# Kernel optimization log

Measured on AMD Instinct MI355X. Metric: run time of the kernel, lower is better.

The kernel has to match this reference:

```python
import jax, jax.numpy as jnp
import numpy as np

EPS = 1e-8
Q_MAX = 127.0  # 2**(8-1) - 1


def _activation_quant(x):
    gamma = jnp.maximum(jnp.max(jnp.abs(x)), EPS)
    scale = Q_MAX / gamma
    x_int = jnp.clip(jnp.round(x * scale), -Q_MAX, Q_MAX)
    x_fq = x_int / scale
    # straight-through estimator
    return x + jax.lax.stop_gradient(x_fq - x)


def _weight_quant(w):
    gamma = jnp.maximum(jnp.mean(jnp.abs(w)), EPS)
    w_int = jnp.clip(jnp.round(w / gamma), -1.0, 1.0)
    w_fq = w_int * gamma
    return w + jax.lax.stop_gradient(w_fq - w)


def setup_inputs() -> dict:
    key = jax.random.key(0)
    kx, kw, kb = jax.random.split(key, 3)
    in_features, out_features = 2048, 2048
    x = jax.random.normal(kx, (4, 4096, in_features), dtype=jnp.float32)
    # nn.Linear default init: U(-1/sqrt(fan_in), 1/sqrt(fan_in))
    bound = 1.0 / np.sqrt(in_features)
    W = jax.random.uniform(kw, (out_features, in_features), dtype=jnp.float32,
                           minval=-bound, maxval=bound)
    b = jax.random.uniform(kb, (out_features,), dtype=jnp.float32,
                           minval=-bound, maxval=bound)
    return {"x": x, "W": W, "b": b}


def reference(x, W, b):
    x_q = _activation_quant(x)          # int8 absmax fake-quant
    w_q = _weight_quant(W)              # ternary {-g, 0, g} fake-quant
    # F.linear: x @ W^T + b
    return jnp.einsum('bsi,oi->bso', x_q, w_q) + b
```

## Files before the change

kernel.cpp:

```cpp
#include <hip/hip_runtime.h>
#include <hip/hip_bf16.h>
#include <stdint.h>

typedef __attribute__((ext_vector_type(4))) int i32x4;

static constexpr long M_ = 16384;
static constexpr long N_ = 2048;
static constexpr long K_ = 2048;


#define GLOAD_LDS16(g, l)                                                          \
  __builtin_amdgcn_global_load_lds(                                               \
      (const __attribute__((address_space(1))) unsigned int*)(g),                 \
      (__attribute__((address_space(3))) unsigned int*)(l), 16, 0, 0)

__global__ __launch_bounds__(256) void k_stats(const float4* __restrict__ x,
                                               const float4* __restrict__ w,
                                               unsigned* __restrict__ gx_bits,
                                               double* __restrict__ gw_sum) {
  const int b = blockIdx.x;
  const int lane = threadIdx.x & 63, wv = threadIdx.x >> 6;
  if (b < 2048) {
    const long S = 524288;
    long i = (long)b * 256 + threadIdx.x;
    float m0 = 0.f, m1 = 0.f, m2 = 0.f, m3 = 0.f;
#pragma unroll
    for (int it = 0; it < 4; ++it) {
      float4 v0 = x[i];
      float4 v1 = x[i + S];
      float4 v2 = x[i + 2 * S];
      float4 v3 = x[i + 3 * S];
      m0 = fmaxf(m0, fmaxf(fmaxf(fabsf(v0.x), fabsf(v0.y)), fmaxf(fabsf(v0.z), fabsf(v0.w))));
      m1 = fmaxf(m1, fmaxf(fmaxf(fabsf(v1.x), fabsf(v1.y)), fmaxf(fabsf(v1.z), fabsf(v1.w))));
      m2 = fmaxf(m2, fmaxf(fmaxf(fabsf(v2.x), fabsf(v2.y)), fmaxf(fabsf(v2.z), fabsf(v2.w))));
      m3 = fmaxf(m3, fmaxf(fmaxf(fabsf(v3.x), fabsf(v3.y)), fmaxf(fabsf(v3.z), fabsf(v3.w))));
      i += 4 * S;
    }
    float m = fmaxf(fmaxf(m0, m1), fmaxf(m2, m3));
#pragma unroll
    for (int off = 32; off > 0; off >>= 1) m = fmaxf(m, __shfl_down(m, off));
    __shared__ float sm[4];
    if (lane == 0) sm[wv] = m;
    __syncthreads();
    if (threadIdx.x == 0) {
      float bm = fmaxf(fmaxf(sm[0], sm[1]), fmaxf(sm[2], sm[3]));
      atomicMax(gx_bits, __float_as_uint(bm));
    }
  } else {
    const long S = 131072;
    long i = (long)(b - 2048) * 256 + threadIdx.x;
    double s = 0.0;
#pragma unroll
    for (int it = 0; it < 8; ++it) {
      float4 v = w[i];
      s += (double)fabsf(v.x) + (double)fabsf(v.y) + (double)fabsf(v.z) + (double)fabsf(v.w);
      i += S;
    }
#pragma unroll
    for (int off = 32; off > 0; off >>= 1) s += __shfl_down(s, off);
    __shared__ double sd[4];
    if (lane == 0) sd[wv] = s;
    __syncthreads();
    if (threadIdx.x == 0) atomicAdd(gw_sum, (sd[0] + sd[1]) + (sd[2] + sd[3]));
  }
}

__global__ __launch_bounds__(256) void k_quant(const float4* __restrict__ x,
                                               const float4* __restrict__ w,
                                               char4* __restrict__ xq,
                                               char4* __restrict__ wq,
                                               const unsigned* __restrict__ gx_bits,
                                               const double* __restrict__ gw_sum) {
  const int b = blockIdx.x;
  if (b < 2048) {
    const double gx = (double)fmaxf(__uint_as_float(*gx_bits), 1e-8f);
    const double scale = 127.0 / gx;
    const long S = 524288;
    long i = (long)b * 256 + threadIdx.x;
#pragma unroll
    for (int it = 0; it < 16; ++it) {
      float4 v = x[i];
      char4 o;
      o.x = (signed char)(int)fmin(fmax(rint((double)v.x * scale), -127.0), 127.0);
      o.y = (signed char)(int)fmin(fmax(rint((double)v.y * scale), -127.0), 127.0);
      o.z = (signed char)(int)fmin(fmax(rint((double)v.z * scale), -127.0), 127.0);
      o.w = (signed char)(int)fmin(fmax(rint((double)v.w * scale), -127.0), 127.0);
      xq[i] = o;
      i += S;
    }
  } else {
    const double gw = fmax(*gw_sum * (1.0 / 4194304.0), 1e-8);
    const double inv = 1.0 / gw;
    const long S = 131072;
    long i = (long)(b - 2048) * 256 + threadIdx.x;
#pragma unroll
    for (int it = 0; it < 8; ++it) {
      float4 v = w[i];
      char4 o;
      o.x = (signed char)(int)fmin(fmax(rint((double)v.x * inv), -1.0), 1.0);
      o.y = (signed char)(int)fmin(fmax(rint((double)v.y * inv), -1.0), 1.0);
      o.z = (signed char)(int)fmin(fmax(rint((double)v.z * inv), -1.0), 1.0);
      o.w = (signed char)(int)fmin(fmax(rint((double)v.w * inv), -1.0), 1.0);
      wq[i] = o;
      i += S;
    }
  }
}


template <int P>
__device__ __forceinline__ void phaseP(signed char* lds, const signed char* Ap,
                                       const signed char* Bp, int kb,
                                       const signed char* pA, const signed char* pB,
                                       int go0, int ldsl0, i32x4 (&aS)[2][4],
                                       i32x4 (&bS)[2][4], i32x4 (&acc)[8][4]) {
  constexpr int Q = (P + 1) & 7;
  constexpr int QR = ((Q >> 2) & 1) * 32768 + ((Q >> 1) & 1) * 16384;
  constexpr int QMH = Q & 1;
#pragma unroll
  for (int m = 0; m < 4; ++m)
    aS[Q & 1][m] = *(const i32x4*)(pA + QR + QMH * 4096 + m * 1024);
  if constexpr (QMH == 0) {
#pragma unroll
    for (int n = 0; n < 4; ++n)
      bS[(Q >> 1) & 1][n] = *(const i32x4*)(pB + QR + n * 1024);
  }
  constexpr int SREG = ((P >> 1) + 3) & 3;
  constexpr int SOFF = ((SREG >> 1) & 1) * 32768 + (SREG & 1) * 16384;
  if constexpr ((P & 1) == 0) {
    GLOAD_LDS16(Ap + kb + go0, lds + SOFF + ldsl0);
    GLOAD_LDS16(Ap + kb + go0 + 32768, lds + SOFF + ldsl0 + 1024);
  } else {
    GLOAD_LDS16(Bp + kb + go0, lds + 65536 + SOFF + ldsl0);
    GLOAD_LDS16(Bp + kb + go0 + 32768, lds + 65536 + SOFF + ldsl0 + 1024);
  }
  __builtin_amdgcn_s_setprio(1);
#pragma unroll
  for (int m = 0; m < 4; ++m)
#pragma unroll
    for (int n = 0; n < 4; ++n)
      acc[(P & 1) * 4 + m][n] = __builtin_amdgcn_mfma_i32_16x16x64_i8(
          aS[P & 1][m], bS[(P >> 1) & 1][n], acc[(P & 1) * 4 + m][n], 0, 0, 0);
  __builtin_amdgcn_s_setprio(0);
  if constexpr ((P & 1) == 1) asm volatile("s_waitcnt vmcnt(4)" ::: "memory");
  __builtin_amdgcn_s_barrier();
}

__global__ __launch_bounds__(512, 2) void k_gemm(
    const signed char* __restrict__ Aq, const signed char* __restrict__ Bq,
    const float* __restrict__ bias, float* __restrict__ out,
    const unsigned* __restrict__ gx_bits, const double* __restrict__ gw_sum) {
  extern __shared__ signed char lds[];

  const int tid = threadIdx.x;
  const int lane = tid & 63;
  const int wid = tid >> 6;
  const int wave_m = wid >> 2;
  const int wave_n = wid & 3;
  const int l15 = lane & 15;

  const int wg = (int)((blockIdx.x & 7) * 64 + (blockIdx.x >> 3));
  const int nblk = wg & 7;
  const int mblk = wg >> 3;
  const long brow = (long)mblk * 256;
  const long bcol = (long)nblk * 256;

  const signed char* Ap = Aq + brow * K_;
  const signed char* Bp = Bq + bcol * K_;

  const int swz = ((lane >> 4) ^ ((l15 >> 1) & 3)) << 4;
  const signed char* pA = lds + (wave_m * 128 + l15) * 64 + swz;
  const signed char* pB = lds + 65536 + (wave_n * 64 + l15) * 64 + swz;

  const int c0 = (lane & 3) ^ ((lane >> 3) & 3);
  const int go0 = (wid * 32 + (lane >> 2)) * (int)K_ + c0 * 16;
  const int ldsl0 = wid * 2048;

  i32x4 acc[8][4];
#pragma unroll
  for (int m = 0; m < 8; m++)
#pragma unroll
    for (int n = 0; n < 4; n++) acc[m][n] = (i32x4){0, 0, 0, 0};
  i32x4 aS[2][4], bS[2][4];

  GLOAD_LDS16(Ap + go0, lds + ldsl0);
  GLOAD_LDS16(Ap + go0 + 32768, lds + ldsl0 + 1024);
  GLOAD_LDS16(Bp + go0, lds + 65536 + ldsl0);
  GLOAD_LDS16(Bp + go0 + 32768, lds + 65536 + ldsl0 + 1024);
  GLOAD_LDS16(Ap + 64 + go0, lds + 16384 + ldsl0);
  GLOAD_LDS16(Ap + 64 + go0 + 32768, lds + 16384 + ldsl0 + 1024);
  GLOAD_LDS16(Bp + 64 + go0, lds + 65536 + 16384 + ldsl0);
  GLOAD_LDS16(Bp + 64 + go0 + 32768, lds + 65536 + 16384 + ldsl0 + 1024);
  GLOAD_LDS16(Ap + 128 + go0, lds + 32768 + ldsl0);
  GLOAD_LDS16(Ap + 128 + go0 + 32768, lds + 32768 + ldsl0 + 1024);
  GLOAD_LDS16(Bp + 128 + go0, lds + 65536 + 32768 + ldsl0);
  GLOAD_LDS16(Bp + 128 + go0 + 32768, lds + 65536 + 32768 + ldsl0 + 1024);
  asm volatile("s_waitcnt vmcnt(0)" ::: "memory");
  __builtin_amdgcn_s_barrier();

#pragma unroll
  for (int n = 0; n < 4; ++n) bS[0][n] = *(const i32x4*)(pB + n * 1024);
#pragma unroll
  for (int m = 0; m < 4; ++m) aS[0][m] = *(const i32x4*)(pA + m * 1024);

  for (int kt = 0; kt < (int)K_; kt += 256) {
    const int c0k = (kt + 192) & 2047;
    const int c1k = (kt + 256) & 2047;
    const int c2k = (kt + 320) & 2047;
    const int c3k = (kt + 384) & 2047;
    phaseP<0>(lds, Ap, Bp, c0k, pA, pB, go0, ldsl0, aS, bS, acc);
    phaseP<1>(lds, Ap, Bp, c0k, pA, pB, go0, ldsl0, aS, bS, acc);
    phaseP<2>(lds, Ap, Bp, c1k, pA, pB, go0, ldsl0, aS, bS, acc);
    phaseP<3>(lds, Ap, Bp, c1k, pA, pB, go0, ldsl0, aS, bS, acc);
    phaseP<4>(lds, Ap, Bp, c2k, pA, pB, go0, ldsl0, aS, bS, acc);
    phaseP<5>(lds, Ap, Bp, c2k, pA, pB, go0, ldsl0, aS, bS, acc);
    phaseP<6>(lds, Ap, Bp, c3k, pA, pB, go0, ldsl0, aS, bS, acc);
    phaseP<7>(lds, Ap, Bp, c3k, pA, pB, go0, ldsl0, aS, bS, acc);
  }

  const float gxf = fmaxf(__uint_as_float(*gx_bits), 1e-8f);
  const double gwd = fmax(*gw_sum * (1.0 / 4194304.0), 1e-8);
  const float alpha = (float)((double)gxf * gwd * (1.0 / 127.0));

#pragma unroll
  for (int n = 0; n < 4; ++n) {
    const long col = bcol + wave_n * 64 + n * 16 + l15;
    const float bv = bias[col];
#pragma unroll
    for (int m = 0; m < 8; ++m) {
      const long row0 = brow + wave_m * 128 + m * 16 + (lane >> 4) * 4;
#pragma unroll
      for (int r = 0; r < 4; ++r) {
        out[(row0 + r) * N_ + col] = (float)acc[m][n][r] * alpha + bv;
      }
    }
  }
}

extern "C" void kernel_launch(void* const* d_in, const int* in_sizes, int n_in,
                              void* d_out, int out_size, void* d_ws, size_t ws_size,
                              hipStream_t stream) {
  const float* x = (const float*)d_in[0];
  const float* W = (const float*)d_in[1];
  const float* b = (const float*)d_in[2];
  float* out = (float*)d_out;

  char* ws = (char*)d_ws;
  double* gw_sum = (double*)ws;
  unsigned* gx_bits = (unsigned*)(ws + 8);
  signed char* xq = (signed char*)(ws + 256);
  signed char* wq = (signed char*)(ws + 256 + (size_t)M_ * (size_t)K_);

  static bool attr_set = false;
  if (!attr_set) {
    (void)hipFuncSetAttribute(reinterpret_cast<const void*>(&k_gemm),
                              hipFuncAttributeMaxDynamicSharedMemorySize, 131072);
    attr_set = true;
  }

  hipMemsetAsync(ws, 0, 16, stream);
  hipLaunchKernelGGL(k_stats, dim3(2560), dim3(256), 0, stream,
                     (const float4*)x, (const float4*)W, gx_bits, gw_sum);
  hipLaunchKernelGGL(k_quant, dim3(2560), dim3(256), 0, stream,
                     (const float4*)x, (const float4*)W, (char4*)xq, (char4*)wq,
                     gx_bits, gw_sum);
  hipLaunchKernelGGL(k_gemm, dim3((unsigned)((M_ / 256) * (N_ / 256))), dim3(512),
                     131072, stream, xq, wq, b, out, gx_bits, gw_sum);
}
```

Before: 156.6 us.

## Load A operand directly from global into registers, stage only B in LDS

The GEMM now reads the int8 activation fragments straight from global memory into registers, addressed per lane, and keeps only the weight tile in LDS. This halves LDS use (131072 to 65536 bytes), removes LDS traffic for A and drops the explicit vmcnt wait. The quant kernel also writes 16-byte vectors of int8 per thread instead of 4-byte char4 stores. The risk is that un-staged A loads are exposed to global latency and are no longer shared across the four waves in a row, raising L2/global traffic; the sync removal and sched_barrier change the ordering of memory and MFMA instructions.

```diff
diff --git a/kernel.cpp b/kernel.cpp
--- a/kernel.cpp
+++ b/kernel.cpp
@@ -67,73 +67,77 @@
 
 __global__ __launch_bounds__(256) void k_quant(const float4* __restrict__ x,
                                                const float4* __restrict__ w,
-                                               char4* __restrict__ xq,
-                                               char4* __restrict__ wq,
+                                               int4* __restrict__ xq,
+                                               int4* __restrict__ wq,
                                                const unsigned* __restrict__ gx_bits,
                                                const double* __restrict__ gw_sum) {
   const int b = blockIdx.x;
   if (b < 2048) {
     const double gx = (double)fmaxf(__uint_as_float(*gx_bits), 1e-8f);
     const double scale = 127.0 / gx;
-    const long S = 524288;
-    long i = (long)b * 256 + threadIdx.x;
-#pragma unroll
-    for (int it = 0; it < 16; ++it) {
-      float4 v = x[i];
-      char4 o;
-      o.x = (signed char)(int)fmin(fmax(rint((double)v.x * scale), -127.0), 127.0);
-      o.y = (signed char)(int)fmin(fmax(rint((double)v.y * scale), -127.0), 127.0);
-      o.z = (signed char)(int)fmin(fmax(rint((double)v.z * scale), -127.0), 127.0);
-      o.w = (signed char)(int)fmin(fmax(rint((double)v.w * scale), -127.0), 127.0);
-      xq[i] = o;
-      i += S;
+    const long G = 2048L * 256;
+    long t = (long)b * 256 + threadIdx.x;
+#pragma unroll
+    for (int it = 0; it < 4; ++it) {
+      signed char o[16];
+#pragma unroll
+      for (int q = 0; q < 4; ++q) {
+        float4 v = x[t * 4 + q];
+        o[q * 4 + 0] = (signed char)(int)fmin(fmax(rint((double)v.x * scale), -127.0), 127.0);
+        o[q * 4 + 1] = (signed char)(int)fmin(fmax(rint((double)v.y * scale), -127.0), 127.0);
+        o[q * 4 + 2] = (signed char)(int)fmin(fmax(rint((double)v.z * scale), -127.0), 127.0);
+        o[q * 4 + 3] = (signed char)(int)fmin(fmax(rint((double)v.w * scale), -127.0), 127.0);
+      }
+      xq[t] = *(const int4*)o;
+      t += G;
     }
   } else {
     const double gw = fmax(*gw_sum * (1.0 / 4194304.0), 1e-8);
     const double inv = 1.0 / gw;
-    const long S = 131072;
-    long i = (long)(b - 2048) * 256 + threadIdx.x;
-#pragma unroll
-    for (int it = 0; it < 8; ++it) {
-      float4 v = w[i];
-      char4 o;
-      o.x = (signed char)(int)fmin(fmax(rint((double)v.x * inv), -1.0), 1.0);
-      o.y = (signed char)(int)fmin(fmax(rint((double)v.y * inv), -1.0), 1.0);
-      o.z = (signed char)(int)fmin(fmax(rint((double)v.z * inv), -1.0), 1.0);
-      o.w = (signed char)(int)fmin(fmax(rint((double)v.w * inv), -1.0), 1.0);
-      wq[i] = o;
-      i += S;
+    const long G = 512L * 256;
+    long t = (long)(b - 2048) * 256 + threadIdx.x;
+#pragma unroll
+    for (int it = 0; it < 2; ++it) {
+      signed char o[16];
+#pragma unroll
+      for (int q = 0; q < 4; ++q) {
+        float4 v = w[t * 4 + q];
+        o[q * 4 + 0] = (signed char)(int)fmin(fmax(rint((double)v.x * inv), -1.0), 1.0);
+        o[q * 4 + 1] = (signed char)(int)fmin(fmax(rint((double)v.y * inv), -1.0), 1.0);
+        o[q * 4 + 2] = (signed char)(int)fmin(fmax(rint((double)v.z * inv), -1.0), 1.0);
+        o[q * 4 + 3] = (signed char)(int)fmin(fmax(rint((double)v.w * inv), -1.0), 1.0);
+      }
+      wq[t] = *(const int4*)o;
+      t += G;
     }
   }
 }
 
 
 template <int P>
-__device__ __forceinline__ void phaseP(signed char* lds, const signed char* Ap,
-                                       const signed char* Bp, int kb,
-                                       const signed char* pA, const signed char* pB,
-                                       int go0, int ldsl0, i32x4 (&aS)[2][4],
-                                       i32x4 (&bS)[2][4], i32x4 (&acc)[8][4]) {
+__device__ __forceinline__ void phaseP(signed char* lds, const signed char* Abase,
+                                       const signed char* Bp, int kA, int kb,
+                                       const signed char* pB, int go0, int ldsl0,
+                                       i32x4 (&aS)[2][4], i32x4 (&bS)[2][4],
+                                       i32x4 (&acc)[8][4]) {
   constexpr int Q = (P + 1) & 7;
-  constexpr int QR = ((Q >> 2) & 1) * 32768 + ((Q >> 1) & 1) * 16384;
   constexpr int QMH = Q & 1;
-#pragma unroll
-  for (int m = 0; m < 4; ++m)
-    aS[Q & 1][m] = *(const i32x4*)(pA + QR + QMH * 4096 + m * 1024);
+  const signed char* pa = Abase + QMH * 131072 + kA;
+#pragma unroll
+  for (int m = 0; m < 4; ++m) aS[Q & 1][m] = *(const i32x4*)(pa + m * 32768);
   if constexpr (QMH == 0) {
+    constexpr int QR = ((Q >> 2) & 1) * 32768 + ((Q >> 1) & 1) * 16384;
 #pragma unroll
     for (int n = 0; n < 4; ++n)
       bS[(Q >> 1) & 1][n] = *(const i32x4*)(pB + QR + n * 1024);
   }
-  constexpr int SREG = ((P >> 1) + 3) & 3;
-  constexpr int SOFF = ((SREG >> 1) & 1) * 32768 + (SREG & 1) * 16384;
   if constexpr ((P & 1) == 0) {
-    GLOAD_LDS16(Ap + kb + go0, lds + SOFF + ldsl0);
-    GLOAD_LDS16(Ap + kb + go0 + 32768, lds + SOFF + ldsl0 + 1024);
-  } else {
-    GLOAD_LDS16(Bp + kb + go0, lds + 65536 + SOFF + ldsl0);
-    GLOAD_LDS16(Bp + kb + go0 + 32768, lds + 65536 + SOFF + ldsl0 + 1024);
-  }
+    constexpr int SREG = ((P >> 1) + 3) & 3;
+    constexpr int SOFF = ((SREG >> 1) & 1) * 32768 + (SREG & 1) * 16384;
+    GLOAD_LDS16(Bp + kb + go0, lds + SOFF + ldsl0);
+    GLOAD_LDS16(Bp + kb + go0 + 32768, lds + SOFF + ldsl0 + 1024);
+  }
+  __builtin_amdgcn_sched_barrier(0);
   __builtin_amdgcn_s_setprio(1);
 #pragma unroll
   for (int m = 0; m < 4; ++m)
@@ -142,7 +146,6 @@
       acc[(P & 1) * 4 + m][n] = __builtin_amdgcn_mfma_i32_16x16x64_i8(
           aS[P & 1][m], bS[(P >> 1) & 1][n], acc[(P & 1) * 4 + m][n], 0, 0, 0);
   __builtin_amdgcn_s_setprio(0);
-  if constexpr ((P & 1) == 1) asm volatile("s_waitcnt vmcnt(4)" ::: "memory");
   __builtin_amdgcn_s_barrier();
 }
 
@@ -165,12 +168,12 @@
   const long brow = (long)mblk * 256;
   const long bcol = (long)nblk * 256;
 
-  const signed char* Ap = Aq + brow * K_;
+  const signed char* Abase =
+      Aq + (brow + wave_m * 128 + l15) * K_ + (lane >> 4) * 16;
   const signed char* Bp = Bq + bcol * K_;
 
   const int swz = ((lane >> 4) ^ ((l15 >> 1) & 3)) << 4;
-  const signed char* pA = lds + (wave_m * 128 + l15) * 64 + swz;
-  const signed char* pB = lds + 65536 + (wave_n * 64 + l15) * 64 + swz;
+  const signed char* pB = lds + (wave_n * 64 + l15) * 64 + swz;
 
   const int c0 = (lane & 3) ^ ((lane >> 3) & 3);
   const int go0 = (wid * 32 + (lane >> 2)) * (int)K_ + c0 * 16;
@@ -183,39 +186,29 @@
     for (int n = 0; n < 4; n++) acc[m][n] = (i32x4){0, 0, 0, 0};
   i32x4 aS[2][4], bS[2][4];
 
-  GLOAD_LDS16(Ap + go0, lds + ldsl0);
-  GLOAD_LDS16(Ap + go0 + 32768, lds + ldsl0 + 1024);
-  GLOAD_LDS16(Bp + go0, lds + 65536 + ldsl0);
-  GLOAD_LDS16(Bp + go0 + 32768, lds + 65536 + ldsl0 + 1024);
-  GLOAD_LDS16(Ap + 64 + go0, lds + 16384 + ldsl0);
-  GLOAD_LDS16(Ap + 64 + go0 + 32768, lds + 16384 + ldsl0 + 1024);
-  GLOAD_LDS16(Bp + 64 + go0, lds + 65536 + 16384 + ldsl0);
-  GLOAD_LDS16(Bp + 64 + go0 + 32768, lds + 65536 + 16384 + ldsl0 + 1024);
-  GLOAD_LDS16(Ap + 128 + go0, lds + 32768 + ldsl0);
-  GLOAD_LDS16(Ap + 128 + go0 + 32768, lds + 32768 + ldsl0 + 1024);
-  GLOAD_LDS16(Bp + 128 + go0, lds + 65536 + 32768 + ldsl0);
-  GLOAD_LDS16(Bp + 128 + go0 + 32768, lds + 65536 + 32768 + ldsl0 + 1024);
+  GLOAD_LDS16(Bp + go0, lds + ldsl0);
+  GLOAD_LDS16(Bp + go0 + 32768, lds + ldsl0 + 1024);
+  GLOAD_LDS16(Bp + 64 + go0, lds + 16384 + ldsl0);
+  GLOAD_LDS16(Bp + 64 + go0 + 32768, lds + 16384 + ldsl0 + 1024);
+  GLOAD_LDS16(Bp + 128 + go0, lds + 32768 + ldsl0);
+  GLOAD_LDS16(Bp + 128 + go0 + 32768, lds + 32768 + ldsl0 + 1024);
   asm volatile("s_waitcnt vmcnt(0)" ::: "memory");
   __builtin_amdgcn_s_barrier();
 
 #pragma unroll
   for (int n = 0; n < 4; ++n) bS[0][n] = *(const i32x4*)(pB + n * 1024);
 #pragma unroll
-  for (int m = 0; m < 4; ++m) aS[0][m] = *(const i32x4*)(pA + m * 1024);
+  for (int m = 0; m < 4; ++m) aS[0][m] = *(const i32x4*)(Abase + m * 32768);
 
   for (int kt = 0; kt < (int)K_; kt += 256) {
-    const int c0k = (kt + 192) & 2047;
-    const int c1k = (kt + 256) & 2047;
-    const int c2k = (kt + 320) & 2047;
-    const int c3k = (kt + 384) & 2047;
-    phaseP<0>(lds, Ap, Bp, c0k, pA, pB, go0, ldsl0, aS, bS, acc);
-    phaseP<1>(lds, Ap, Bp, c0k, pA, pB, go0, ldsl0, aS, bS, acc);
-    phaseP<2>(lds, Ap, Bp, c1k, pA, pB, go0, ldsl0, aS, bS, acc);
-    phaseP<3>(lds, Ap, Bp, c1k, pA, pB, go0, ldsl0, aS, bS, acc);
-    phaseP<4>(lds, Ap, Bp, c2k, pA, pB, go0, ldsl0, aS, bS, acc);
-    phaseP<5>(lds, Ap, Bp, c2k, pA, pB, go0, ldsl0, aS, bS, acc);
-    phaseP<6>(lds, Ap, Bp, c3k, pA, pB, go0, ldsl0, aS, bS, acc);
-    phaseP<7>(lds, Ap, Bp, c3k, pA, pB, go0, ldsl0, aS, bS, acc);
+    phaseP<0>(lds, Abase, Bp, (kt + 0) & 2047, (kt + 192) & 2047, pB, go0, ldsl0, aS, bS, acc);
+    phaseP<1>(lds, Abase, Bp, (kt + 64) & 2047, 0, pB, go0, ldsl0, aS, bS, acc);
+    phaseP<2>(lds, Abase, Bp, (kt + 64) & 2047, (kt + 256) & 2047, pB, go0, ldsl0, aS, bS, acc);
+    phaseP<3>(lds, Abase, Bp, (kt + 128) & 2047, 0, pB, go0, ldsl0, aS, bS, acc);
+    phaseP<4>(lds, Abase, Bp, (kt + 128) & 2047, (kt + 320) & 2047, pB, go0, ldsl0, aS, bS, acc);
+    phaseP<5>(lds, Abase, Bp, (kt + 192) & 2047, 0, pB, go0, ldsl0, aS, bS, acc);
+    phaseP<6>(lds, Abase, Bp, (kt + 192) & 2047, (kt + 384) & 2047, pB, go0, ldsl0, aS, bS, acc);
+    phaseP<7>(lds, Abase, Bp, (kt + 256) & 2047, 0, pB, go0, ldsl0, aS, bS, acc);
   }
 
   const float gxf = fmaxf(__uint_as_float(*gx_bits), 1e-8f);
@@ -254,7 +247,7 @@
   static bool attr_set = false;
   if (!attr_set) {
     (void)hipFuncSetAttribute(reinterpret_cast<const void*>(&k_gemm),
-                              hipFuncAttributeMaxDynamicSharedMemorySize, 131072);
+                              hipFuncAttributeMaxDynamicSharedMemorySize, 65536);
     attr_set = true;
   }
 
@@ -262,8 +255,8 @@
   hipLaunchKernelGGL(k_stats, dim3(2560), dim3(256), 0, stream,
                      (const float4*)x, (const float4*)W, gx_bits, gw_sum);
   hipLaunchKernelGGL(k_quant, dim3(2560), dim3(256), 0, stream,
-                     (const float4*)x, (const float4*)W, (char4*)xq, (char4*)wq,
+                     (const float4*)x, (const float4*)W, (int4*)xq, (int4*)wq,
                      gx_bits, gw_sum);
   hipLaunchKernelGGL(k_gemm, dim3((unsigned)((M_ / 256) * (N_ / 256))), dim3(512),
-                     131072, stream, xq, wq, b, out, gx_bits, gw_sum);
-}
+                     65536, stream, xq, wq, b, out, gx_bits, gw_sum);
+}
```

Measured after the change: 240.1 us. 1.53x slower.
